# Kernel optimization log

Hardware: AMD Instinct MI355X
Metric: run time of the kernel (lower is better)

## Reference

```python
import jax, jax.numpy as jnp
import numpy as np

DIM = 2048
RANK = 16
NUM_EXPERTS = 8


def setup_inputs() -> dict:
    key = jax.random.key(0)
    ks = jax.random.split(key, 8)
    x = jax.random.normal(ks[0], (4, 2048, DIM), dtype=jnp.float32)
    # router gate: nn.Linear(dim, num_experts) -> weight [E, dim], bias [E]
    gate_w = jax.random.normal(ks[1], (NUM_EXPERTS, DIM), dtype=jnp.float32) * 0.02
    gate_b = jnp.zeros((NUM_EXPERTS,), dtype=jnp.float32)
    # base_ffn: nn.Linear(dim, dim) -> weight [dim, dim], bias [dim]
    base_w = jax.random.normal(ks[2], (DIM, DIM), dtype=jnp.float32) * 0.02
    base_b = jnp.zeros((DIM,), dtype=jnp.float32)
    # LoRA experts, stacked: A maps dim->rank, B maps rank->dim (stored input-major)
    lora_A = jax.random.normal(ks[3], (NUM_EXPERTS, DIM, RANK), dtype=jnp.float32) * 0.02
    lora_B = jax.random.normal(ks[4], (NUM_EXPERTS, RANK, DIM), dtype=jnp.float32) * 0.02
    return {"x": x, "gate_w": gate_w, "gate_b": gate_b,
            "base_w": base_w, "base_b": base_b,
            "lora_A": lora_A, "lora_B": lora_B}


def reference(x, gate_w, gate_b, base_w, base_b, lora_A, lora_B):
    B, S, D = x.shape
    flat = x.reshape(-1, D)  # [T, D]
    # base FFN: Linear + exact GELU (torch default)
    base_out = jax.nn.gelu(flat @ base_w.T + base_b, approximate=False)
    # router: softmax then top-1
    probs = jax.nn.softmax(flat @ gate_w.T + gate_b, axis=-1)  # [T, E]
    idx = jnp.argmax(probs, axis=-1)                            # [T] top-1 index
    w = jnp.take_along_axis(probs, idx[:, None], axis=-1)      # [T, 1] top-1 weight
    E = lora_A.shape[0]
    expert_out = jnp.zeros_like(flat)
    for e in range(E):  # fixed small expert loop; GEMMs are dense over all tokens
        h = jax.nn.gelu(flat @ lora_A[e], approximate=False)   # [T, rank]
        ye = h @ lora_B[e]                                      # [T, D]
        sel = (idx == e)[:, None]
        expert_out = expert_out + jnp.where(sel, ye * w, 0.0)
    out = (base_out + expert_out).reshape(B, S, D)
    return out, probs
```

## Files before the change

kernel.cpp:

```cpp
#include <hip/hip_runtime.h>
#include <hip/hip_bf16.h>
#include <math.h>


#define DIM   2048
#define RANK  16
#define NEXP  8
#define NTOK  8192
#define KLORA 128

typedef __hip_bfloat16 bf16;
typedef __attribute__((ext_vector_type(8))) short short8;
typedef __attribute__((ext_vector_type(4))) float float4v;

typedef const __attribute__((address_space(1))) void* gptr_t;
typedef __attribute__((address_space(3))) void*       sptr_t;

__device__ __forceinline__ void async_ld16(const bf16* g, bf16* l) {
    __builtin_amdgcn_global_load_lds((gptr_t)g, (sptr_t)l, 16, 0, 0);
}

__device__ __forceinline__ float gelu_fast(float x) {
    float t = 0.7978845608028654f * (x + 0.044715f * x * x * x);
    t = fminf(fmaxf(t, -10.0f), 10.0f);
    float e = __expf(2.0f * t);
    float th = (e - 1.0f) / (e + 1.0f);
    return 0.5f * x * (1.0f + th);
}

__device__ __forceinline__ short8 pack8(float4 v0, float4 v1) {
    union { bf16 h[8]; short8 v; } u;
    u.h[0] = __float2bfloat16(v0.x); u.h[1] = __float2bfloat16(v0.y);
    u.h[2] = __float2bfloat16(v0.z); u.h[3] = __float2bfloat16(v0.w);
    u.h[4] = __float2bfloat16(v1.x); u.h[5] = __float2bfloat16(v1.y);
    u.h[6] = __float2bfloat16(v1.z); u.h[7] = __float2bfloat16(v1.w);
    return u.v;
}

__global__ __launch_bounds__(256) void cvt_logits_kernel(
    const float* __restrict__ x, const float* __restrict__ gate_w,
    const float* __restrict__ gate_b, const float* __restrict__ base_w,
    const float* __restrict__ lora_B, const float* __restrict__ lora_A,
    bf16* __restrict__ Xb, bf16* __restrict__ Wb,
    bf16* __restrict__ Bt, bf16* __restrict__ Ab,
    float* __restrict__ probs, int* __restrict__ idx_out, float* __restrict__ w_out)
{
    __shared__ float buf[2560];
    const int b   = blockIdx.x;
    const int tid = threadIdx.x;

    if (b < NTOK) {
        const float* xr = x + (size_t)b * DIM + tid * 8;
        float4 v0 = *(const float4*)xr;
        float4 v1 = *(const float4*)(xr + 4);
        *(short8*)(Xb + (size_t)b * DIM + tid * 8) = pack8(v0, v1);

        float acc[NEXP];
        #pragma unroll
        for (int e = 0; e < NEXP; e++) {
            const float* wr = gate_w + (size_t)e * DIM + tid * 8;
            float4 w0 = *(const float4*)wr;
            float4 w1 = *(const float4*)(wr + 4);
            acc[e] = v0.x * w0.x + v0.y * w0.y + v0.z * w0.z + v0.w * w0.w
                   + v1.x * w1.x + v1.y * w1.y + v1.z * w1.z + v1.w * w1.w;
        }
        #pragma unroll
        for (int e = 0; e < NEXP; e++) {
            #pragma unroll
            for (int off = 32; off > 0; off >>= 1)
                acc[e] += __shfl_down(acc[e], off);
        }
        const int wave = tid >> 6, lane = tid & 63;
        if (lane == 0) {
            #pragma unroll
            for (int e = 0; e < NEXP; e++) buf[wave * NEXP + e] = acc[e];
        }
        __syncthreads();
        if (tid == 0) {
            float l[NEXP]; float mx = -1e30f;
            #pragma unroll
            for (int e = 0; e < NEXP; e++) {
                l[e] = buf[e] + buf[8 + e] + buf[16 + e] + buf[24 + e] + gate_b[e];
                mx = fmaxf(mx, l[e]);
            }
            float sum = 0.f;
            #pragma unroll
            for (int e = 0; e < NEXP; e++) { l[e] = __expf(l[e] - mx); sum += l[e]; }
            float inv = 1.0f / sum;
            int es = 0; float best = l[0];
            #pragma unroll
            for (int e = 1; e < NEXP; e++) if (l[e] > best) { best = l[e]; es = e; }
            #pragma unroll
            for (int e = 0; e < NEXP; e++) probs[(size_t)b * NEXP + e] = l[e] * inv;
            idx_out[b] = es;
            w_out[b]   = best * inv;
        }
    } else if (b < NTOK + 2048) {
        size_t v = ((size_t)(b - NTOK) * 256 + tid) * 8;
        float4 v0 = *(const float4*)(base_w + v);
        float4 v1 = *(const float4*)(base_w + v + 4);
        *(short8*)(Wb + v) = pack8(v0, v1);
    } else if (b < NTOK + 2048 + 256) {
        int bb = b - NTOK - 2048;
        int kk0 = (bb >> 6) * 32, j0 = (bb & 63) * 32;
        {
            int r = tid >> 3, c4 = (tid & 7) * 4;
            float4 val = *(const float4*)(lora_B + (size_t)(kk0 + r) * DIM + j0 + c4);
            *(float4*)(buf + r * 36 + c4) = val;
        }
        __syncthreads();
        {
            int j = tid >> 3, k4 = (tid & 7) * 4;
            bf16* dst = Bt + (size_t)(j0 + j) * KLORA + kk0 + k4;
            #pragma unroll
            for (int i = 0; i < 4; i++) dst[i] = __float2bfloat16(buf[(k4 + i) * 36 + j]);
        }
    } else {
        int bb = b - NTOK - 2048 - 256;
        int e = bb >> 4, k0 = (bb & 15) * 128;
        const float* src = lora_A + (size_t)e * DIM * RANK;
        {
            int k = tid >> 2, r4 = (tid & 3) * 4;
            float4 va = *(const float4*)(src + (size_t)(k0 + k) * RANK + r4);
            float4 vb = *(const float4*)(src + (size_t)(k0 + k + 64) * RANK + r4);
            *(float4*)(buf + k * 20 + r4)        = va;
            *(float4*)(buf + (k + 64) * 20 + r4) = vb;
        }
        __syncthreads();
        {
            int r = tid >> 4, kx = (tid & 15) * 8;
            bf16* dst = Ab + (size_t)(e * 16 + r) * DIM + k0 + kx;
            #pragma unroll
            for (int i = 0; i < 8; i++) dst[i] = __float2bfloat16(buf[(kx + i) * 20 + r]);
        }
    }
}

__global__ __launch_bounds__(256) void hsel_kernel(
    const bf16* __restrict__ Xb, const bf16* __restrict__ Ab,
    const int* __restrict__ idx, const float* __restrict__ wsel,
    bf16* __restrict__ A2)
{
    __shared__ bf16 As[32 * 32];
    __shared__ bf16 Bs[64 * 32];
    const int tid  = threadIdx.x;
    const int wave = tid >> 6, lane = tid & 63;
    const int m0 = blockIdx.x * 32;
    const int n0 = blockIdx.y * 64;
    const int col = lane & 15, quad = lane >> 4;

    const int kc = ((tid & 3) ^ ((tid >> 3) & 3)) * 8;
    const bf16* gB = Ab + (size_t)(n0 + (tid >> 2)) * DIM + kc;
    const bf16* gA = Xb + (size_t)(m0 + (tid >> 2)) * DIM + kc;
    bf16* lB = Bs + wave * 512;
    bf16* lA = As + wave * 512;

    const int xr = quad ^ ((col >> 1) & 3);
    const bf16* pa = As + col * 32 + xr * 8;
    const bf16* pb = Bs + (wave * 16 + col) * 32 + xr * 8;

    float4v acc[2] = {};
    for (int k0 = 0; k0 < DIM; k0 += 32) {
        __syncthreads();
        async_ld16(gB + k0, lB);
        if (tid < 128) async_ld16(gA + k0, lA);
        __syncthreads();
        short8 a0 = *(const short8*)pa;
        short8 a1 = *(const short8*)(pa + 512);
        short8 b0 = *(const short8*)pb;
        acc[0] = __builtin_amdgcn_mfma_f32_16x16x32_bf16(a0, b0, acc[0], 0, 0, 0);
        acc[1] = __builtin_amdgcn_mfma_f32_16x16x32_bf16(a1, b0, acc[1], 0, 0, 0);
    }

    const int jcol = n0 + wave * 16 + col;
    const int ej   = jcol >> 4;
    #pragma unroll
    for (int i = 0; i < 2; i++) {
        int rbase = m0 + i * 16 + quad * 4;
        #pragma unroll
        for (int r = 0; r < 4; r++) {
            int t = rbase + r;
            float v = (idx[t] == ej) ? gelu_fast(acc[i][r]) * wsel[t] : 0.0f;
            A2[(size_t)t * KLORA + jcol] = __float2bfloat16(v);
        }
    }
}

__global__ __launch_bounds__(256, 3) void gemm_kernel(
    const bf16* __restrict__ Xb, const bf16* __restrict__ Wb,
    const float* __restrict__ base_b,
    const bf16* __restrict__ A2, const bf16* __restrict__ Bt,
    float* __restrict__ out)
{
    __shared__ bf16 As[128 * 32];
    __shared__ bf16 Bs[128 * 32];
    const int tid  = threadIdx.x;
    const int wave = tid >> 6, lane = tid & 63;
    const int wm = wave >> 1, wn = wave & 1;
    const int m0 = blockIdx.x * 128;
    const int n0 = blockIdx.y * 128;
    const int col = lane & 15, quad = lane >> 4;

    const int kc = ((tid & 3) ^ ((tid >> 3) & 3)) * 8;
    const bf16* gA0 = Xb + (size_t)(m0 + (tid >> 2)) * DIM + kc;
    const bf16* gB0 = Wb + (size_t)(n0 + (tid >> 2)) * DIM + kc;
    const bf16* gA1 = gA0 + (size_t)64 * DIM;
    const bf16* gB1 = gB0 + (size_t)64 * DIM;
    bf16* lA0 = As + wave * 512;
    bf16* lA1 = lA0 + 2048;
    bf16* lB0 = Bs + wave * 512;
    bf16* lB1 = lB0 + 2048;

    const int xr = quad ^ ((col >> 1) & 3);
    const bf16* pa = As + (wm * 64 + col) * 32 + xr * 8;
    const bf16* pb = Bs + (wn * 64 + col) * 32 + xr * 8;

    float4v acc[4][4] = {};

    for (int k0 = 0; k0 < DIM; k0 += 32) {
        __syncthreads();
        async_ld16(gA0 + k0, lA0);
        async_ld16(gA1 + k0, lA1);
        async_ld16(gB0 + k0, lB0);
        async_ld16(gB1 + k0, lB1);
        __syncthreads();
        short8 a[4], b[4];
        #pragma unroll
        for (int i = 0; i < 4; i++) a[i] = *(const short8*)(pa + i * 512);
        #pragma unroll
        for (int j = 0; j < 4; j++) b[j] = *(const short8*)(pb + j * 512);
        #pragma unroll
        for (int i = 0; i < 4; i++)
            #pragma unroll
            for (int j = 0; j < 4; j++)
                acc[i][j] = __builtin_amdgcn_mfma_f32_16x16x32_bf16(
                    a[i], b[j], acc[i][j], 0, 0, 0);
    }

    float bias[4];
    #pragma unroll
    for (int j = 0; j < 4; j++) bias[j] = base_b[n0 + wn * 64 + j * 16 + col];
    #pragma unroll
    for (int i = 0; i < 4; i++)
        #pragma unroll
        for (int j = 0; j < 4; j++)
            #pragma unroll
            for (int r = 0; r < 4; r++)
                acc[i][j][r] = gelu_fast(acc[i][j][r] + bias[j]);

    const bf16* pea = A2 + (size_t)(m0 + wm * 64 + col) * KLORA + quad * 8;
    const bf16* peb = Bt + (size_t)(n0 + wn * 64 + col) * KLORA + quad * 8;
    #pragma unroll
    for (int ks = 0; ks < 4; ks++) {
        short8 ea[4], eb[4];
        #pragma unroll
        for (int i = 0; i < 4; i++)
            ea[i] = *(const short8*)(pea + i * 16 * KLORA + ks * 32);
        #pragma unroll
        for (int j = 0; j < 4; j++)
            eb[j] = *(const short8*)(peb + j * 16 * KLORA + ks * 32);
        #pragma unroll
        for (int i = 0; i < 4; i++)
            #pragma unroll
            for (int j = 0; j < 4; j++)
                acc[i][j] = __builtin_amdgcn_mfma_f32_16x16x32_bf16(
                    ea[i], eb[j], acc[i][j], 0, 0, 0);
    }

    #pragma unroll
    for (int i = 0; i < 4; i++) {
        #pragma unroll
        for (int j = 0; j < 4; j++) {
            int tt = m0 + wm * 64 + i * 16 + quad * 4;
            int jj = n0 + wn * 64 + j * 16 + col;
            float* po = out + (size_t)tt * DIM + jj;
            #pragma unroll
            for (int r = 0; r < 4; r++) po[(size_t)r * DIM] = acc[i][j][r];
        }
    }
}

extern "C" void kernel_launch(void* const* d_in, const int* in_sizes, int n_in,
                              void* d_out, int out_size, void* d_ws, size_t ws_size,
                              hipStream_t stream)
{
    (void)in_sizes; (void)n_in; (void)out_size; (void)ws_size;
    const float* x      = (const float*)d_in[0];
    const float* gate_w = (const float*)d_in[1];
    const float* gate_b = (const float*)d_in[2];
    const float* base_w = (const float*)d_in[3];
    const float* base_b = (const float*)d_in[4];
    const float* lora_A = (const float*)d_in[5];
    const float* lora_B = (const float*)d_in[6];

    float* out   = (float*)d_out;
    float* probs = out + (size_t)NTOK * DIM;

    char* ws = (char*)d_ws;
    bf16*  Xb   = (bf16*)ws;
    bf16*  Wb   = (bf16*)(ws + 33554432);
    bf16*  A2   = (bf16*)(ws + 41943040);
    bf16*  Bt   = (bf16*)(ws + 44040192);
    bf16*  Ab   = (bf16*)(ws + 44564480);
    int*   idx  = (int*) (ws + 45088768);
    float* wsel = (float*)(ws + 45121536);

    cvt_logits_kernel<<<NTOK + 2048 + 256 + 128, 256, 0, stream>>>(
        x, gate_w, gate_b, base_w, lora_B, lora_A,
        Xb, Wb, Bt, Ab, probs, idx, wsel);
    hsel_kernel<<<dim3(256, 2), 256, 0, stream>>>(Xb, Ab, idx, wsel, A2);
    gemm_kernel<<<dim3(64, 16), 256, 0, stream>>>(Xb, Wb, base_b, A2, Bt, out);
}
```

Before: 297.1 us.

## Batch router tokens per block and deepen GEMM K-tile to 64 with swizzled LDS

The conversion/router kernel now handles 8 tokens per block, so gate weights are loaded once and reused across tokens instead of once per token, which cuts the block count. The main GEMM's K step grows from 32 to 64, with an 8-way XOR swizzle on the LDS layout, which halves the number of barrier pairs per tile. The grid is also reordered so blocks sharing an M row run adjacently, which changes L2 reuse. The larger LDS footprint may reduce occupancy.

```diff
diff --git a/kernel.cpp b/kernel.cpp
--- a/kernel.cpp
+++ b/kernel.cpp
@@ -49,38 +49,44 @@
     const int b   = blockIdx.x;
     const int tid = threadIdx.x;
 
-    if (b < NTOK) {
-        const float* xr = x + (size_t)b * DIM + tid * 8;
-        float4 v0 = *(const float4*)xr;
-        float4 v1 = *(const float4*)(xr + 4);
-        *(short8*)(Xb + (size_t)b * DIM + tid * 8) = pack8(v0, v1);
-
-        float acc[NEXP];
+    if (b < 1024) {
+        const int t0 = b * 8;
+        float4 g0[NEXP], g1[NEXP];
         #pragma unroll
         for (int e = 0; e < NEXP; e++) {
             const float* wr = gate_w + (size_t)e * DIM + tid * 8;
-            float4 w0 = *(const float4*)wr;
-            float4 w1 = *(const float4*)(wr + 4);
-            acc[e] = v0.x * w0.x + v0.y * w0.y + v0.z * w0.z + v0.w * w0.w
-                   + v1.x * w1.x + v1.y * w1.y + v1.z * w1.z + v1.w * w1.w;
-        }
-        #pragma unroll
-        for (int e = 0; e < NEXP; e++) {
-            #pragma unroll
-            for (int off = 32; off > 0; off >>= 1)
-                acc[e] += __shfl_down(acc[e], off);
+            g0[e] = *(const float4*)wr;
+            g1[e] = *(const float4*)(wr + 4);
         }
         const int wave = tid >> 6, lane = tid & 63;
-        if (lane == 0) {
-            #pragma unroll
-            for (int e = 0; e < NEXP; e++) buf[wave * NEXP + e] = acc[e];
-        }
-        __syncthreads();
-        if (tid == 0) {
+        #pragma unroll
+        for (int tt = 0; tt < 8; tt++) {
+            const int t = t0 + tt;
+            const float* xr = x + (size_t)t * DIM + tid * 8;
+            float4 v0 = *(const float4*)xr;
+            float4 v1 = *(const float4*)(xr + 4);
+            *(short8*)(Xb + (size_t)t * DIM + tid * 8) = pack8(v0, v1);
+            float a[NEXP];
+            #pragma unroll
+            for (int e = 0; e < NEXP; e++) {
+                a[e] = v0.x * g0[e].x + v0.y * g0[e].y + v0.z * g0[e].z + v0.w * g0[e].w
+                     + v1.x * g1[e].x + v1.y * g1[e].y + v1.z * g1[e].z + v1.w * g1[e].w;
+                #pragma unroll
+                for (int off = 32; off > 0; off >>= 1) a[e] += __shfl_down(a[e], off);
+            }
+            if (lane == 0) {
+                #pragma unroll
+                for (int e = 0; e < NEXP; e++) buf[tt * 32 + wave * NEXP + e] = a[e];
+            }
+        }
+        __syncthreads();
+        if (tid < 8) {
+            const int t = t0 + tid;
             float l[NEXP]; float mx = -1e30f;
             #pragma unroll
             for (int e = 0; e < NEXP; e++) {
-                l[e] = buf[e] + buf[8 + e] + buf[16 + e] + buf[24 + e] + gate_b[e];
+                l[e] = buf[tid * 32 + e] + buf[tid * 32 + 8 + e]
+                     + buf[tid * 32 + 16 + e] + buf[tid * 32 + 24 + e] + gate_b[e];
                 mx = fmaxf(mx, l[e]);
             }
             float sum = 0.f;
@@ -91,17 +97,17 @@
             #pragma unroll
             for (int e = 1; e < NEXP; e++) if (l[e] > best) { best = l[e]; es = e; }
             #pragma unroll
-            for (int e = 0; e < NEXP; e++) probs[(size_t)b * NEXP + e] = l[e] * inv;
-            idx_out[b] = es;
-            w_out[b]   = best * inv;
-        }
-    } else if (b < NTOK + 2048) {
-        size_t v = ((size_t)(b - NTOK) * 256 + tid) * 8;
+            for (int e = 0; e < NEXP; e++) probs[(size_t)t * NEXP + e] = l[e] * inv;
+            idx_out[t] = es;
+            w_out[t]   = best * inv;
+        }
+    } else if (b < 1024 + 2048) {
+        size_t v = ((size_t)(b - 1024) * 256 + tid) * 8;
         float4 v0 = *(const float4*)(base_w + v);
         float4 v1 = *(const float4*)(base_w + v + 4);
         *(short8*)(Wb + v) = pack8(v0, v1);
-    } else if (b < NTOK + 2048 + 256) {
-        int bb = b - NTOK - 2048;
+    } else if (b < 1024 + 2048 + 256) {
+        int bb = b - 1024 - 2048;
         int kk0 = (bb >> 6) * 32, j0 = (bb & 63) * 32;
         {
             int r = tid >> 3, c4 = (tid & 7) * 4;
@@ -116,7 +122,7 @@
             for (int i = 0; i < 4; i++) dst[i] = __float2bfloat16(buf[(k4 + i) * 36 + j]);
         }
     } else {
-        int bb = b - NTOK - 2048 - 256;
+        int bb = b - 1024 - 2048 - 256;
         int e = bb >> 4, k0 = (bb & 15) * 128;
         const float* src = lora_A + (size_t)e * DIM * RANK;
         {
@@ -192,49 +198,72 @@
     const bf16* __restrict__ A2, const bf16* __restrict__ Bt,
     float* __restrict__ out)
 {
-    __shared__ bf16 As[128 * 32];
-    __shared__ bf16 Bs[128 * 32];
+    __shared__ bf16 As[128 * 64];
+    __shared__ bf16 Bs[128 * 64];
     const int tid  = threadIdx.x;
     const int wave = tid >> 6, lane = tid & 63;
     const int wm = wave >> 1, wn = wave & 1;
-    const int m0 = blockIdx.x * 128;
-    const int n0 = blockIdx.y * 128;
+    const int n0 = blockIdx.x * 128;
+    const int m0 = blockIdx.y * 128;
     const int col = lane & 15, quad = lane >> 4;
 
-    const int kc = ((tid & 3) ^ ((tid >> 3) & 3)) * 8;
-    const bf16* gA0 = Xb + (size_t)(m0 + (tid >> 2)) * DIM + kc;
-    const bf16* gB0 = Wb + (size_t)(n0 + (tid >> 2)) * DIM + kc;
-    const bf16* gA1 = gA0 + (size_t)64 * DIM;
-    const bf16* gB1 = gB0 + (size_t)64 * DIM;
-    bf16* lA0 = As + wave * 512;
-    bf16* lA1 = lA0 + 2048;
-    bf16* lB0 = Bs + wave * 512;
-    bf16* lB1 = lB0 + 2048;
-
-    const int xr = quad ^ ((col >> 1) & 3);
-    const bf16* pa = As + (wm * 64 + col) * 32 + xr * 8;
-    const bf16* pb = Bs + (wn * 64 + col) * 32 + xr * 8;
+    const int kc = (((tid & 7) ^ ((tid >> 3) & 7))) * 8;
+    const int r0 = tid >> 3;
+    const bf16* gA0 = Xb + (size_t)(m0 + r0) * DIM + kc;
+    const bf16* gB0 = Wb + (size_t)(n0 + r0) * DIM + kc;
+    const bf16* gA1 = gA0 + (size_t)32 * DIM;
+    const bf16* gB1 = gB0 + (size_t)32 * DIM;
+    const bf16* gA2 = gA0 + (size_t)64 * DIM;
+    const bf16* gB2 = gB0 + (size_t)64 * DIM;
+    const bf16* gA3 = gA0 + (size_t)96 * DIM;
+    const bf16* gB3 = gB0 + (size_t)96 * DIM;
+    bf16* lA = As + wave * 512;
+    bf16* lB = Bs + wave * 512;
+
+    const int sl0 = (quad        ^ (col & 7)) * 8;
+    const int sl1 = ((quad | 4)  ^ (col & 7)) * 8;
+    const bf16* paA = As + (wm * 64 + col) * 64;
+    const bf16* pbB = Bs + (wn * 64 + col) * 64;
 
     float4v acc[4][4] = {};
 
-    for (int k0 = 0; k0 < DIM; k0 += 32) {
-        __syncthreads();
-        async_ld16(gA0 + k0, lA0);
-        async_ld16(gA1 + k0, lA1);
-        async_ld16(gB0 + k0, lB0);
-        async_ld16(gB1 + k0, lB1);
-        __syncthreads();
-        short8 a[4], b[4];
-        #pragma unroll
-        for (int i = 0; i < 4; i++) a[i] = *(const short8*)(pa + i * 512);
-        #pragma unroll
-        for (int j = 0; j < 4; j++) b[j] = *(const short8*)(pb + j * 512);
-        #pragma unroll
-        for (int i = 0; i < 4; i++)
-            #pragma unroll
-            for (int j = 0; j < 4; j++)
-                acc[i][j] = __builtin_amdgcn_mfma_f32_16x16x32_bf16(
-                    a[i], b[j], acc[i][j], 0, 0, 0);
+    for (int k0 = 0; k0 < DIM; k0 += 64) {
+        __syncthreads();
+        async_ld16(gA0 + k0, lA);
+        async_ld16(gA1 + k0, lA + 2048);
+        async_ld16(gA2 + k0, lA + 4096);
+        async_ld16(gA3 + k0, lA + 6144);
+        async_ld16(gB0 + k0, lB);
+        async_ld16(gB1 + k0, lB + 2048);
+        async_ld16(gB2 + k0, lB + 4096);
+        async_ld16(gB3 + k0, lB + 6144);
+        __syncthreads();
+        {
+            short8 a[4], b[4];
+            #pragma unroll
+            for (int i = 0; i < 4; i++) a[i] = *(const short8*)(paA + i * 1024 + sl0);
+            #pragma unroll
+            for (int j = 0; j < 4; j++) b[j] = *(const short8*)(pbB + j * 1024 + sl0);
+            #pragma unroll
+            for (int i = 0; i < 4; i++)
+                #pragma unroll
+                for (int j = 0; j < 4; j++)
+                    acc[i][j] = __builtin_amdgcn_mfma_f32_16x16x32_bf16(
+                        a[i], b[j], acc[i][j], 0, 0, 0);
+        }
+        {
+            short8 a[4], b[4];
+            #pragma unroll
+            for (int i = 0; i < 4; i++) a[i] = *(const short8*)(paA + i * 1024 + sl1);
+            #pragma unroll
+            for (int j = 0; j < 4; j++) b[j] = *(const short8*)(pbB + j * 1024 + sl1);
+            #pragma unroll
+            for (int i = 0; i < 4; i++)
+                #pragma unroll
+                for (int j = 0; j < 4; j++)
+                    acc[i][j] = __builtin_amdgcn_mfma_f32_16x16x32_bf16(
+                        a[i], b[j], acc[i][j], 0, 0, 0);
+        }
     }
 
     float bias[4];
@@ -305,9 +334,9 @@
     int*   idx  = (int*) (ws + 45088768);
     float* wsel = (float*)(ws + 45121536);
 
-    cvt_logits_kernel<<<NTOK + 2048 + 256 + 128, 256, 0, stream>>>(
+    cvt_logits_kernel<<<1024 + 2048 + 256 + 128, 256, 0, stream>>>(
         x, gate_w, gate_b, base_w, lora_B, lora_A,
         Xb, Wb, Bt, Ab, probs, idx, wsel);
     hsel_kernel<<<dim3(256, 2), 256, 0, stream>>>(Xb, Ab, idx, wsel, A2);
-    gemm_kernel<<<dim3(64, 16), 256, 0, stream>>>(Xb, Wb, base_b, A2, Bt, out);
-}
+    gemm_kernel<<<dim3(16, 64), 256, 0, stream>>>(Xb, Wb, base_b, A2, Bt, out);
+}
```

Result: faster. 253.2 us (-14.8%).
